# Optimization experiments

Measured on AMD Instinct MI355X. Metric: run time of the kernel, lower is better.

Reference implementation:

```python
import jax, jax.numpy as jnp
import numpy as np

D = 8  # polynomial degree; with bias present, basis has D columns (P1..PD)


def setup_inputs() -> dict:
    key = jax.random.key(0)
    k1, k2 = jax.random.split(key)
    batch, n_in, n_out = 65536, 256, 64
    x = jax.random.normal(k1, (batch, n_in), dtype=jnp.float32)
    c_basis = jax.random.normal(k2, (n_out, n_in, D), dtype=jnp.float32) * (1.0 / np.sqrt(n_in * D))
    bias = jnp.zeros((n_out,), dtype=jnp.float32)
    return {"x": x, "c_basis": c_basis, "bias": bias}


def _legendre_basis(x):
    # x: (batch, n_in). Returns (batch, n_in, D) = [P1(t), ..., PD(t)], t = tanh(x).
    t = jnp.tanh(x)
    p_prev = jnp.ones_like(t)  # P0
    p_curr = t                 # P1
    polys = [p_curr]
    for k in range(2, D + 1):  # small fixed-length loop over degree
        p_next = ((2 * k - 1) * t * p_curr - (k - 1) * p_prev) / k
        polys.append(p_next)
        p_prev, p_curr = p_curr, p_next
    return jnp.stack(polys, axis=-1)  # (batch, n_in, D)


def reference(x, c_basis, bias):
    # basis: (batch, n_in, D); contract over (n_in, D) with c_basis (n_out, n_in, D)
    leg = _legendre_basis(x)
    y = jnp.einsum('bid,oid->bo', leg, c_basis)
    return y + bias
```

## Files before the change

### kernel.cpp

```cpp
#include <hip/hip_runtime.h>
#include <hip/hip_bf16.h>

typedef __attribute__((ext_vector_type(8))) short short8;
typedef __attribute__((ext_vector_type(4))) float floatx4;
typedef __attribute__((ext_vector_type(4))) unsigned int uintx4;

__device__ __forceinline__ unsigned pack2_bf16_rn(float a, float b) {
  __hip_bfloat162 h = __float22bfloat162_rn(make_float2(a, b));
  unsigned r;
  __builtin_memcpy(&r, &h, 4);
  return r;
}

__device__ __forceinline__ unsigned pack2_bf16_fast(float a, float b) {
  unsigned ua, ub;
  __builtin_memcpy(&ua, &a, 4);
  __builtin_memcpy(&ub, &b, 4);
  return __builtin_amdgcn_perm(ub + 0x8000u, ua + 0x8000u, 0x07060302u);
}

__device__ __forceinline__ short8 legendre_frag(float xv) {
  float e  = __builtin_amdgcn_exp2f(xv * 2.885390081777927f);
  float t  = 1.0f - 2.0f * __builtin_amdgcn_rcpf(e + 1.0f);
  float p1 = t;
  float u2 = t * p1,  w2 = u2 - 1.0f;        float p2 = fmaf(0.5f, w2, u2);
  float u3 = t * p2,  w3 = u3 - p1;          float p3 = fmaf(2.0f/3.0f, w3, u3);
  float u4 = t * p3,  w4 = u4 - p2;          float p4 = fmaf(0.75f, w4, u4);
  float u5 = t * p4,  w5 = u5 - p3;          float p5 = fmaf(0.8f, w5, u5);
  float u6 = t * p5,  w6 = u6 - p4;          float p6 = fmaf(5.0f/6.0f, w6, u6);
  float u7 = t * p6,  w7 = u7 - p5;          float p7 = fmaf(6.0f/7.0f, w7, u7);
  float u8 = t * p7,  w8 = u8 - p6;          float p8 = fmaf(7.0f/8.0f, w8, u8);
  union { unsigned u[4]; short8 s; } r;
  r.u[0] = pack2_bf16_fast(p1, p2);
  r.u[1] = pack2_bf16_fast(p3, p4);
  r.u[2] = pack2_bf16_fast(p5, p6);
  r.u[3] = pack2_bf16_fast(p7, p8);
  return r.s;
}

__global__ void conv_kernel(const float* __restrict__ cb, unsigned short* __restrict__ ws) {
  int t = blockIdx.x * 256 + threadIdx.x;
  int o = t & 63;
  int i = t >> 6;
  const floatx4* s = (const floatx4*)(cb + ((size_t)o * 256 + i) * 8);
  floatx4 v0 = s[0], v1 = s[1];
  uintx4 w;
  w.x = pack2_bf16_rn(v0.x, v0.y);
  w.y = pack2_bf16_rn(v0.z, v0.w);
  w.z = pack2_bf16_rn(v1.x, v1.y);
  w.w = pack2_bf16_rn(v1.z, v1.w);
  *(uintx4*)(ws + (size_t)i * 512 + o * 8) = w;
}

__global__ __launch_bounds__(128, 2) void kan_kernel(
    const float* __restrict__ x, const unsigned short* __restrict__ ws,
    const float* __restrict__ bias, float* __restrict__ y) {
  const int tid  = threadIdx.x;
  const int wid  = tid >> 6;
  const int lane = tid & 63;
  const int m    = lane & 15;
  const int q    = lane >> 4;
  const int row_block = blockIdx.x * 64;

  floatx4 acc[2][4];
#pragma unroll
  for (int a = 0; a < 2; ++a)
#pragma unroll
    for (int nt = 0; nt < 4; ++nt) acc[a][nt] = (floatx4){0.f, 0.f, 0.f, 0.f};

  const int r0g = row_block + wid * 32 + m;
  const float* xp0 = x + (size_t)r0g * 256 + q;
  const float* xp1 = xp0 + 16 * 256;
  const unsigned short* bp = ws + q * 512 + m * 8;

  short8 fbN[4];
#pragma unroll
  for (int nt = 0; nt < 4; ++nt) fbN[nt] = *(const short8*)(bp + nt * 128);
  float xvN0 = xp0[0];
  float xvN1 = xp1[0];

#pragma unroll 2
  for (int s = 0; s < 64; ++s) {
    short8 fb0 = fbN[0], fb1 = fbN[1], fb2 = fbN[2], fb3 = fbN[3];
    float xv0 = xvN0, xv1 = xvN1;
    int sn = (s < 63) ? (s + 1) : 63;
#pragma unroll
    for (int nt = 0; nt < 4; ++nt)
      fbN[nt] = *(const short8*)(bp + (size_t)sn * 2048 + nt * 128);
    xvN0 = xp0[sn * 4];
    xvN1 = xp1[sn * 4];

    short8 fa0 = legendre_frag(xv0);
    short8 fa1 = legendre_frag(xv1);
    acc[0][0] = __builtin_amdgcn_mfma_f32_16x16x32_bf16(fa0, fb0, acc[0][0], 0, 0, 0);
    acc[1][0] = __builtin_amdgcn_mfma_f32_16x16x32_bf16(fa1, fb0, acc[1][0], 0, 0, 0);
    acc[0][1] = __builtin_amdgcn_mfma_f32_16x16x32_bf16(fa0, fb1, acc[0][1], 0, 0, 0);
    acc[1][1] = __builtin_amdgcn_mfma_f32_16x16x32_bf16(fa1, fb1, acc[1][1], 0, 0, 0);
    acc[0][2] = __builtin_amdgcn_mfma_f32_16x16x32_bf16(fa0, fb2, acc[0][2], 0, 0, 0);
    acc[1][2] = __builtin_amdgcn_mfma_f32_16x16x32_bf16(fa1, fb2, acc[1][2], 0, 0, 0);
    acc[0][3] = __builtin_amdgcn_mfma_f32_16x16x32_bf16(fa0, fb3, acc[0][3], 0, 0, 0);
    acc[1][3] = __builtin_amdgcn_mfma_f32_16x16x32_bf16(fa1, fb3, acc[1][3], 0, 0, 0);
  }

  float bv[4];
#pragma unroll
  for (int nt = 0; nt < 4; ++nt) bv[nt] = bias[nt * 16 + m];
#pragma unroll
  for (int a = 0; a < 2; ++a) {
    int gr0 = row_block + wid * 32 + a * 16 + q * 4;
#pragma unroll
    for (int nt = 0; nt < 4; ++nt) {
#pragma unroll
      for (int r = 0; r < 4; ++r) {
        y[(size_t)(gr0 + r) * 64 + nt * 16 + m] = acc[a][nt][r] + bv[nt];
      }
    }
  }
}

extern "C" void kernel_launch(void* const* d_in, const int* in_sizes, int n_in,
                              void* d_out, int out_size, void* d_ws, size_t ws_size,
                              hipStream_t stream) {
  const float* x    = (const float*)d_in[0];
  const float* cb   = (const float*)d_in[1];
  const float* bias = (const float*)d_in[2];
  float* y = (float*)d_out;
  unsigned short* ws = (unsigned short*)d_ws;
  int batch = in_sizes[0] / 256;
  hipLaunchKernelGGL(conv_kernel, dim3(64), dim3(256), 0, stream, cb, ws);
  hipLaunchKernelGGL(kan_kernel, dim3(batch / 64), dim3(128), 0, stream, x, ws, bias, y);
}
```

Baseline: 139.8 us.

## Split K across two waves per block with LDS reduction and deeper prefetch

```diff
diff --git a/kernel.cpp b/kernel.cpp
--- a/kernel.cpp
+++ b/kernel.cpp
@@ -23,13 +23,13 @@
   float e  = __builtin_amdgcn_exp2f(xv * 2.885390081777927f);
   float t  = 1.0f - 2.0f * __builtin_amdgcn_rcpf(e + 1.0f);
   float p1 = t;
-  float u2 = t * p1,  w2 = u2 - 1.0f;        float p2 = fmaf(0.5f, w2, u2);
-  float u3 = t * p2,  w3 = u3 - p1;          float p3 = fmaf(2.0f/3.0f, w3, u3);
-  float u4 = t * p3,  w4 = u4 - p2;          float p4 = fmaf(0.75f, w4, u4);
-  float u5 = t * p4,  w5 = u5 - p3;          float p5 = fmaf(0.8f, w5, u5);
-  float u6 = t * p5,  w6 = u6 - p4;          float p6 = fmaf(5.0f/6.0f, w6, u6);
-  float u7 = t * p6,  w7 = u7 - p5;          float p7 = fmaf(6.0f/7.0f, w7, u7);
-  float u8 = t * p7,  w8 = u8 - p6;          float p8 = fmaf(7.0f/8.0f, w8, u8);
+  float u2 = t * p1,  w2 = u2 - 1.0f;  float p2 = fmaf(0.5f, w2, u2);
+  float u3 = t * p2,  w3 = u3 - p1;    float p3 = fmaf(2.0f/3.0f, w3, u3);
+  float u4 = t * p3,  w4 = u4 - p2;    float p4 = fmaf(0.75f, w4, u4);
+  float u5 = t * p4,  w5 = u5 - p3;    float p5 = fmaf(0.8f, w5, u5);
+  float u6 = t * p5,  w6 = u6 - p4;    float p6 = fmaf(5.0f/6.0f, w6, u6);
+  float u7 = t * p6,  w7 = u7 - p5;    float p7 = fmaf(6.0f/7.0f, w7, u7);
+  float u8 = t * p7,  w8 = u8 - p6;    float p8 = fmaf(7.0f/8.0f, w8, u8);
   union { unsigned u[4]; short8 s; } r;
   r.u[0] = pack2_bf16_fast(p1, p2);
   r.u[1] = pack2_bf16_fast(p3, p4);
@@ -52,15 +52,19 @@
   *(uintx4*)(ws + (size_t)i * 512 + o * 8) = w;
 }
 
-__global__ __launch_bounds__(128, 2) void kan_kernel(
+#define ITERS 32
+
+__global__ __launch_bounds__(128, 4) void kan_kernel(
     const float* __restrict__ x, const unsigned short* __restrict__ ws,
     const float* __restrict__ bias, float* __restrict__ y) {
+  __shared__ floatx4 red[8 * 64];
+
   const int tid  = threadIdx.x;
   const int wid  = tid >> 6;
   const int lane = tid & 63;
   const int m    = lane & 15;
   const int q    = lane >> 4;
-  const int row_block = blockIdx.x * 64;
+  const int row_block = blockIdx.x * 32;
 
   floatx4 acc[2][4];
 #pragma unroll
@@ -68,51 +72,73 @@
 #pragma unroll
     for (int nt = 0; nt < 4; ++nt) acc[a][nt] = (floatx4){0.f, 0.f, 0.f, 0.f};
 
-  const int r0g = row_block + wid * 32 + m;
-  const float* xp0 = x + (size_t)r0g * 256 + q;
+  const int r0g = row_block + m;
+  const float* xp0 = x + (size_t)r0g * 256 + (size_t)wid * 128 + q;
   const float* xp1 = xp0 + 16 * 256;
-  const unsigned short* bp = ws + q * 512 + m * 8;
+  const unsigned short* bp = ws + (size_t)wid * 32 * 2048 + q * 512 + m * 8;
 
-  short8 fbN[4];
+  short8 fb[3][4];
+  float xq0[4], xq1[4];
 #pragma unroll
-  for (int nt = 0; nt < 4; ++nt) fbN[nt] = *(const short8*)(bp + nt * 128);
-  float xvN0 = xp0[0];
-  float xvN1 = xp1[0];
-
-#pragma unroll 2
-  for (int s = 0; s < 64; ++s) {
-    short8 fb0 = fbN[0], fb1 = fbN[1], fb2 = fbN[2], fb3 = fbN[3];
-    float xv0 = xvN0, xv1 = xvN1;
-    int sn = (s < 63) ? (s + 1) : 63;
+  for (int sp = 0; sp < 2; ++sp)
 #pragma unroll
     for (int nt = 0; nt < 4; ++nt)
-      fbN[nt] = *(const short8*)(bp + (size_t)sn * 2048 + nt * 128);
-    xvN0 = xp0[sn * 4];
-    xvN1 = xp1[sn * 4];
+      fb[sp][nt] = *(const short8*)(bp + (size_t)sp * 2048 + nt * 128);
+#pragma unroll
+  for (int sp = 0; sp < 4; ++sp) {
+    xq0[sp] = xp0[sp * 4];
+    xq1[sp] = xp1[sp * 4];
+  }
+
+#pragma unroll
+  for (int s = 0; s < ITERS; ++s) {
+    float xv0 = xq0[s & 3];
+    float xv1 = xq1[s & 3];
+    if (s + 2 < ITERS) {
+#pragma unroll
+      for (int nt = 0; nt < 4; ++nt)
+        fb[(s + 2) % 3][nt] = *(const short8*)(bp + (size_t)(s + 2) * 2048 + nt * 128);
+    }
+    if (s + 4 < ITERS) {
+      xq0[s & 3] = xp0[(s + 4) * 4];
+      xq1[s & 3] = xp1[(s + 4) * 4];
+    }
 
     short8 fa0 = legendre_frag(xv0);
     short8 fa1 = legendre_frag(xv1);
-    acc[0][0] = __builtin_amdgcn_mfma_f32_16x16x32_bf16(fa0, fb0, acc[0][0], 0, 0, 0);
-    acc[1][0] = __builtin_amdgcn_mfma_f32_16x16x32_bf16(fa1, fb0, acc[1][0], 0, 0, 0);
-    acc[0][1] = __builtin_amdgcn_mfma_f32_16x16x32_bf16(fa0, fb1, acc[0][1], 0, 0, 0);
-    acc[1][1] = __builtin_amdgcn_mfma_f32_16x16x32_bf16(fa1, fb1, acc[1][1], 0, 0, 0);
-    acc[0][2] = __builtin_amdgcn_mfma_f32_16x16x32_bf16(fa0, fb2, acc[0][2], 0, 0, 0);
-    acc[1][2] = __builtin_amdgcn_mfma_f32_16x16x32_bf16(fa1, fb2, acc[1][2], 0, 0, 0);
-    acc[0][3] = __builtin_amdgcn_mfma_f32_16x16x32_bf16(fa0, fb3, acc[0][3], 0, 0, 0);
-    acc[1][3] = __builtin_amdgcn_mfma_f32_16x16x32_bf16(fa1, fb3, acc[1][3], 0, 0, 0);
+    const int b = s % 3;
+    acc[0][0] = __builtin_amdgcn_mfma_f32_16x16x32_bf16(fa0, fb[b][0], acc[0][0], 0, 0, 0);
+    acc[1][0] = __builtin_amdgcn_mfma_f32_16x16x32_bf16(fa1, fb[b][0], acc[1][0], 0, 0, 0);
+    acc[0][1] = __builtin_amdgcn_mfma_f32_16x16x32_bf16(fa0, fb[b][1], acc[0][1], 0, 0, 0);
+    acc[1][1] = __builtin_amdgcn_mfma_f32_16x16x32_bf16(fa1, fb[b][1], acc[1][1], 0, 0, 0);
+    acc[0][2] = __builtin_amdgcn_mfma_f32_16x16x32_bf16(fa0, fb[b][2], acc[0][2], 0, 0, 0);
+    acc[1][2] = __builtin_amdgcn_mfma_f32_16x16x32_bf16(fa1, fb[b][2], acc[1][2], 0, 0, 0);
+    acc[0][3] = __builtin_amdgcn_mfma_f32_16x16x32_bf16(fa0, fb[b][3], acc[0][3], 0, 0, 0);
+    acc[1][3] = __builtin_amdgcn_mfma_f32_16x16x32_bf16(fa1, fb[b][3], acc[1][3], 0, 0, 0);
   }
 
-  float bv[4];
+  if (wid == 1) {
 #pragma unroll
-  for (int nt = 0; nt < 4; ++nt) bv[nt] = bias[nt * 16 + m];
+    for (int a = 0; a < 2; ++a)
 #pragma unroll
-  for (int a = 0; a < 2; ++a) {
-    int gr0 = row_block + wid * 32 + a * 16 + q * 4;
+      for (int nt = 0; nt < 4; ++nt)
+        red[(a * 4 + nt) * 64 + lane] = acc[a][nt];
+  }
+  __syncthreads();
+  if (wid == 0) {
+    float bv[4];
 #pragma unroll
-    for (int nt = 0; nt < 4; ++nt) {
+    for (int nt = 0; nt < 4; ++nt) bv[nt] = bias[nt * 16 + m];
 #pragma unroll
-      for (int r = 0; r < 4; ++r) {
-        y[(size_t)(gr0 + r) * 64 + nt * 16 + m] = acc[a][nt][r] + bv[nt];
+    for (int a = 0; a < 2; ++a) {
+      int gr0 = row_block + a * 16 + q * 4;
+#pragma unroll
+      for (int nt = 0; nt < 4; ++nt) {
+        floatx4 p = red[(a * 4 + nt) * 64 + lane];
+#pragma unroll
+        for (int r = 0; r < 4; ++r) {
+          y[(size_t)(gr0 + r) * 64 + nt * 16 + m] = acc[a][nt][r] + p[r] + bv[nt];
+        }
       }
     }
   }
@@ -128,5 +154,5 @@
   unsigned short* ws = (unsigned short*)d_ws;
   int batch = in_sizes[0] / 256;
   hipLaunchKernelGGL(conv_kernel, dim3(64), dim3(256), 0, stream, cb, ws);
-  hipLaunchKernelGGL(kan_kernel, dim3(batch / 64), dim3(128), 0, stream, x, ws, bias, y);
+  hipLaunchKernelGGL(kan_kernel, dim3(batch / 32), dim3(128), 0, stream, x, ws, bias, y);
 }
```

Result: no change. 139.9 us (+0.0%).

## Stage weights and x through LDS with async double-buffered global-to-LDS loads

Applied to the files above, without the earlier changes.

```diff
diff --git a/kernel.cpp b/kernel.cpp
--- a/kernel.cpp
+++ b/kernel.cpp
@@ -4,6 +4,14 @@
 typedef __attribute__((ext_vector_type(8))) short short8;
 typedef __attribute__((ext_vector_type(4))) float floatx4;
 typedef __attribute__((ext_vector_type(4))) unsigned int uintx4;
+
+#define GLOBAL_AS __attribute__((address_space(1)))
+#define LDS_AS __attribute__((address_space(3)))
+
+__device__ __forceinline__ void async_ld16(const void* g, void* l) {
+  __builtin_amdgcn_global_load_lds((const GLOBAL_AS unsigned int*)g,
+                                   (LDS_AS unsigned int*)l, 16, 0, 0);
+}
 
 __device__ __forceinline__ unsigned pack2_bf16_rn(float a, float b) {
   __hip_bfloat162 h = __float22bfloat162_rn(make_float2(a, b));
@@ -23,13 +31,13 @@
   float e  = __builtin_amdgcn_exp2f(xv * 2.885390081777927f);
   float t  = 1.0f - 2.0f * __builtin_amdgcn_rcpf(e + 1.0f);
   float p1 = t;
-  float u2 = t * p1,  w2 = u2 - 1.0f;        float p2 = fmaf(0.5f, w2, u2);
-  float u3 = t * p2,  w3 = u3 - p1;          float p3 = fmaf(2.0f/3.0f, w3, u3);
-  float u4 = t * p3,  w4 = u4 - p2;          float p4 = fmaf(0.75f, w4, u4);
-  float u5 = t * p4,  w5 = u5 - p3;          float p5 = fmaf(0.8f, w5, u5);
-  float u6 = t * p5,  w6 = u6 - p4;          float p6 = fmaf(5.0f/6.0f, w6, u6);
-  float u7 = t * p6,  w7 = u7 - p5;          float p7 = fmaf(6.0f/7.0f, w7, u7);
-  float u8 = t * p7,  w8 = u8 - p6;          float p8 = fmaf(7.0f/8.0f, w8, u8);
+  float u2 = t * p1,  w2 = u2 - 1.0f;  float p2 = fmaf(0.5f, w2, u2);
+  float u3 = t * p2,  w3 = u3 - p1;    float p3 = fmaf(2.0f/3.0f, w3, u3);
+  float u4 = t * p3,  w4 = u4 - p2;    float p4 = fmaf(0.75f, w4, u4);
+  float u5 = t * p4,  w5 = u5 - p3;    float p5 = fmaf(0.8f, w5, u5);
+  float u6 = t * p5,  w6 = u6 - p4;    float p6 = fmaf(5.0f/6.0f, w6, u6);
+  float u7 = t * p6,  w7 = u7 - p5;    float p7 = fmaf(6.0f/7.0f, w7, u7);
+  float u8 = t * p7,  w8 = u8 - p6;    float p8 = fmaf(7.0f/8.0f, w8, u8);
   union { unsigned u[4]; short8 s; } r;
   r.u[0] = pack2_bf16_fast(p1, p2);
   r.u[1] = pack2_bf16_fast(p3, p4);
@@ -40,8 +48,8 @@
 
 __global__ void conv_kernel(const float* __restrict__ cb, unsigned short* __restrict__ ws) {
   int t = blockIdx.x * 256 + threadIdx.x;
-  int o = t & 63;
-  int i = t >> 6;
+  int o = t >> 8;
+  int i = t & 255;
   const floatx4* s = (const floatx4*)(cb + ((size_t)o * 256 + i) * 8);
   floatx4 v0 = s[0], v1 = s[1];
   uintx4 w;
@@ -52,15 +60,21 @@
   *(uintx4*)(ws + (size_t)i * 512 + o * 8) = w;
 }
 
-__global__ __launch_bounds__(128, 2) void kan_kernel(
+#define MB 128
+#define NCH 16
+
+__global__ __launch_bounds__(256, 2) void kan_kernel(
     const float* __restrict__ x, const unsigned short* __restrict__ ws,
     const float* __restrict__ bias, float* __restrict__ y) {
+  __shared__ __align__(16) unsigned short bt[2][16 * 64 * 8];
+  __shared__ __align__(16) float xs[2][MB * 16];
+
   const int tid  = threadIdx.x;
   const int wid  = tid >> 6;
   const int lane = tid & 63;
   const int m    = lane & 15;
   const int q    = lane >> 4;
-  const int row_block = blockIdx.x * 64;
+  const int row_block = blockIdx.x * MB;
 
   floatx4 acc[2][4];
 #pragma unroll
@@ -68,38 +82,58 @@
 #pragma unroll
     for (int nt = 0; nt < 4; ++nt) acc[a][nt] = (floatx4){0.f, 0.f, 0.f, 0.f};
 
-  const int r0g = row_block + wid * 32 + m;
-  const float* xp0 = x + (size_t)r0g * 256 + q;
-  const float* xp1 = xp0 + 16 * 256;
-  const unsigned short* bp = ws + q * 512 + m * 8;
+  auto stage = [&](int ch, int buf) {
+#pragma unroll
+    for (int t = 0; t < 4; ++t) {
+      int sb = t * 256 + wid * 64;
+      async_ld16(ws + (size_t)ch * 8192 + (size_t)(sb + lane) * 8, &bt[buf][sb * 8]);
+    }
+#pragma unroll
+    for (int t = 0; t < 2; ++t) {
+      int sb = t * 256 + wid * 64;
+      int slot = sb + lane;
+      int r = slot >> 2;
+      int c4 = (slot & 3) ^ (r & 3);
+      async_ld16(x + (size_t)(row_block + r) * 256 + ch * 16 + c4 * 4, &xs[buf][sb * 4]);
+    }
+  };
 
-  short8 fbN[4];
+  const int xoff0 = (wid * 32 + m) * 64 + ((m & 3) << 4) + q * 4;
+  const int xoff1 = xoff0 + 16 * 64;
+
+  stage(0, 0);
+#pragma unroll 2
+  for (int ch = 0; ch < NCH; ++ch) {
+    const int buf = ch & 1;
+    asm volatile("s_barrier" ::: "memory");
+    if (ch + 1 < NCH) {
+      stage(ch + 1, buf ^ 1);
+      asm volatile("s_waitcnt vmcnt(6)" ::: "memory");
+    } else {
+      asm volatile("s_waitcnt vmcnt(0)" ::: "memory");
+    }
+
+    const unsigned short* bp = &bt[buf][q * 512 + m * 8];
+    const char* xb = (const char*)&xs[buf][0];
 #pragma unroll
-  for (int nt = 0; nt < 4; ++nt) fbN[nt] = *(const short8*)(bp + nt * 128);
-  float xvN0 = xp0[0];
-  float xvN1 = xp1[0];
-
-#pragma unroll 2
-  for (int s = 0; s < 64; ++s) {
-    short8 fb0 = fbN[0], fb1 = fbN[1], fb2 = fbN[2], fb3 = fbN[3];
-    float xv0 = xvN0, xv1 = xvN1;
-    int sn = (s < 63) ? (s + 1) : 63;
-#pragma unroll
-    for (int nt = 0; nt < 4; ++nt)
-      fbN[nt] = *(const short8*)(bp + (size_t)sn * 2048 + nt * 128);
-    xvN0 = xp0[sn * 4];
-    xvN1 = xp1[sn * 4];
-
-    short8 fa0 = legendre_frag(xv0);
-    short8 fa1 = legendre_frag(xv1);
-    acc[0][0] = __builtin_amdgcn_mfma_f32_16x16x32_bf16(fa0, fb0, acc[0][0], 0, 0, 0);
-    acc[1][0] = __builtin_amdgcn_mfma_f32_16x16x32_bf16(fa1, fb0, acc[1][0], 0, 0, 0);
-    acc[0][1] = __builtin_amdgcn_mfma_f32_16x16x32_bf16(fa0, fb1, acc[0][1], 0, 0, 0);
-    acc[1][1] = __builtin_amdgcn_mfma_f32_16x16x32_bf16(fa1, fb1, acc[1][1], 0, 0, 0);
-    acc[0][2] = __builtin_amdgcn_mfma_f32_16x16x32_bf16(fa0, fb2, acc[0][2], 0, 0, 0);
-    acc[1][2] = __builtin_amdgcn_mfma_f32_16x16x32_bf16(fa1, fb2, acc[1][2], 0, 0, 0);
-    acc[0][3] = __builtin_amdgcn_mfma_f32_16x16x32_bf16(fa0, fb3, acc[0][3], 0, 0, 0);
-    acc[1][3] = __builtin_amdgcn_mfma_f32_16x16x32_bf16(fa1, fb3, acc[1][3], 0, 0, 0);
+    for (int ks = 0; ks < 4; ++ks) {
+      short8 fb0 = *(const short8*)(bp + ks * 2048 + 0 * 128);
+      short8 fb1 = *(const short8*)(bp + ks * 2048 + 1 * 128);
+      short8 fb2 = *(const short8*)(bp + ks * 2048 + 2 * 128);
+      short8 fb3 = *(const short8*)(bp + ks * 2048 + 3 * 128);
+      float xv0 = *(const float*)(xb + (xoff0 ^ (ks << 4)));
+      float xv1 = *(const float*)(xb + (xoff1 ^ (ks << 4)));
+      short8 fa0 = legendre_frag(xv0);
+      short8 fa1 = legendre_frag(xv1);
+      acc[0][0] = __builtin_amdgcn_mfma_f32_16x16x32_bf16(fa0, fb0, acc[0][0], 0, 0, 0);
+      acc[1][0] = __builtin_amdgcn_mfma_f32_16x16x32_bf16(fa1, fb0, acc[1][0], 0, 0, 0);
+      acc[0][1] = __builtin_amdgcn_mfma_f32_16x16x32_bf16(fa0, fb1, acc[0][1], 0, 0, 0);
+      acc[1][1] = __builtin_amdgcn_mfma_f32_16x16x32_bf16(fa1, fb1, acc[1][1], 0, 0, 0);
+      acc[0][2] = __builtin_amdgcn_mfma_f32_16x16x32_bf16(fa0, fb2, acc[0][2], 0, 0, 0);
+      acc[1][2] = __builtin_amdgcn_mfma_f32_16x16x32_bf16(fa1, fb2, acc[1][2], 0, 0, 0);
+      acc[0][3] = __builtin_amdgcn_mfma_f32_16x16x32_bf16(fa0, fb3, acc[0][3], 0, 0, 0);
+      acc[1][3] = __builtin_amdgcn_mfma_f32_16x16x32_bf16(fa1, fb3, acc[1][3], 0, 0, 0);
+    }
   }
 
   float bv[4];
@@ -128,5 +162,5 @@
   unsigned short* ws = (unsigned short*)d_ws;
   int batch = in_sizes[0] / 256;
   hipLaunchKernelGGL(conv_kernel, dim3(64), dim3(256), 0, stream, cb, ws);
-  hipLaunchKernelGGL(kan_kernel, dim3(batch / 64), dim3(128), 0, stream, x, ws, bias, y);
+  hipLaunchKernelGGL(kan_kernel, dim3(batch / MB), dim3(256), 0, stream, x, ws, bias, y);
 }
```

Measured after the change: 123.3 us. 1.13x faster.
